# Kernel optimization log

Hardware: AMD Instinct MI355X
Metric: run time of the kernel (lower is better)

The kernel has to match this reference:

```python
import jax, jax.numpy as jnp
import numpy as np

B, S, DIM, H, DH = 1, 4096, 2048, 16, 128
EPS = 1e-5


def setup_inputs() -> dict:
    key = jax.random.key(0)
    ks = jax.random.split(key, 16)
    sc = 0.02
    inp = {
        'hidden_states': jax.random.normal(ks[0], (B, S, DIM), jnp.float32),
        'freqs_cos': jax.random.uniform(ks[1], (1, S, 1, DH), jnp.float32),
        'freqs_sin': jax.random.uniform(ks[2], (1, S, 1, DH), jnp.float32),
        'Wq': jax.random.normal(ks[3], (DIM, DIM), jnp.float32) * sc,
        'bq': jax.random.normal(ks[4], (DIM,), jnp.float32) * sc,
        'Wk': jax.random.normal(ks[5], (DIM, DIM), jnp.float32) * sc,
        'bk': jax.random.normal(ks[6], (DIM,), jnp.float32) * sc,
        'Wv': jax.random.normal(ks[7], (DIM, DIM), jnp.float32) * sc,
        'bv': jax.random.normal(ks[8], (DIM,), jnp.float32) * sc,
        'Wo': jax.random.normal(ks[9], (DIM, DIM), jnp.float32) * sc,
        'bo': jax.random.normal(ks[10], (DIM,), jnp.float32) * sc,
        'gq': jnp.ones((DIM,), jnp.float32),
        'gk': jnp.ones((DIM,), jnp.float32),
    }
    return inp


def _rmsnorm(x, g):
    var = jnp.mean(jnp.square(x), axis=-1, keepdims=True)
    return x * jax.lax.rsqrt(var + EPS) * g


def _apply_rope(x, freqs_cos, freqs_sin):
    # x: [B,S,H,DH]; interleaved rotary as in WanAttnProcessor
    x1 = x[..., 0::2]
    x2 = x[..., 1::2]
    cos = freqs_cos[..., 0::2]
    sin = freqs_sin[..., 1::2]
    o1 = x1 * cos - x2 * sin
    o2 = x1 * sin + x2 * cos
    return jnp.stack([o1, o2], axis=-1).reshape(x.shape)


def reference(hidden_states, freqs_cos, freqs_sin, Wq, bq, Wk, bk, Wv, bv, Wo, bo, gq, gk):
    q = hidden_states @ Wq + bq
    k = hidden_states @ Wk + bk
    v = hidden_states @ Wv + bv
    q = _rmsnorm(q, gq)
    k = _rmsnorm(k, gk)
    q = q.reshape(B, S, H, DH)
    k = k.reshape(B, S, H, DH)
    v = v.reshape(B, S, H, DH)
    q = _apply_rope(q, freqs_cos, freqs_sin)
    k = _apply_rope(k, freqs_cos, freqs_sin)
    scale = 1.0 / np.sqrt(DH).astype(np.float32)
    scores = jnp.einsum('bqhd,bkhd->bhqk', q, k) * scale
    attn = jax.nn.softmax(scores, axis=-1)
    out = jnp.einsum('bhqk,bkhd->bqhd', attn, v)
    out = out.reshape(B, S, H * DH)
    return out @ Wo + bo
```

## Files before the change

### kernel.cpp

```cpp
#include <hip/hip_runtime.h>
#include <hip/hip_bf16.h>

#define SEQ 4096
#define DIMC 2048
#define NH 16
#define DHD 128

typedef short s8v __attribute__((ext_vector_type(8)));
typedef float f4v __attribute__((ext_vector_type(4)));
typedef __bf16 bf8 __attribute__((ext_vector_type(8)));
typedef float f4 __attribute__((ext_vector_type(4)));
typedef float f16v __attribute__((ext_vector_type(16)));
typedef int i4v __attribute__((ext_vector_type(4)));

typedef __attribute__((address_space(3))) void lds_t;
typedef __attribute__((address_space(1))) void gbl_t;

__device__ __attribute__((aligned(256))) short g_h[(size_t)SEQ * DIMC];
__device__ __attribute__((aligned(256))) short g_q[(size_t)SEQ * DIMC];
__device__ __attribute__((aligned(256))) short g_k[(size_t)SEQ * DIMC];
__device__ __attribute__((aligned(256))) short g_v[(size_t)SEQ * DIMC];
__device__ __attribute__((aligned(256))) short g_vt[(size_t)DIMC * SEQ];
__device__ __attribute__((aligned(256))) short g_wt[4][(size_t)DIMC * DIMC];

__device__ __forceinline__ float b2f(short s) {
    union { unsigned u; float f; } v;
    v.u = ((unsigned)(unsigned short)s) << 16;
    return v.f;
}
__device__ __forceinline__ short f2b(float f) {
    union { float f; unsigned u; } v;
    v.f = f;
    unsigned b = v.u;
    b += 0x7FFFu + ((b >> 16) & 1u);
    return (short)(b >> 16);
}
__device__ __forceinline__ f4 mfma16(bf8 a, bf8 b, f4 c) {
    return __builtin_amdgcn_mfma_f32_16x16x32_bf16(a, b, c, 0, 0, 0);
}
__device__ __forceinline__ f16v mfma32(bf8 a, bf8 b, f16v c) {
    return __builtin_amdgcn_mfma_f32_32x32x16_bf16(a, b, c, 0, 0, 0);
}
__device__ __forceinline__ void gl_lds16(const short* g, short* l) {
    __builtin_amdgcn_global_load_lds((gbl_t*)g, (lds_t*)l, 16, 0, 0);
}
__device__ __forceinline__ void plane32_swap(int& a, int& b) {
    asm("v_permlane32_swap_b32 %0, %1" : "+v"(a), "+v"(b));
}
__device__ __forceinline__ int pk2b(float a, float b) {
    int r;
    asm("v_cvt_pk_bf16_f32 %0, %1, %2" : "=v"(r) : "v"(a), "v"(b));
    return r;
}
__device__ __forceinline__ float fexp2(float x) {
#if __has_builtin(__builtin_amdgcn_exp2f)
    return __builtin_amdgcn_exp2f(x);
#else
    float r;
    asm("v_exp_f32 %0, %1" : "=v"(r) : "v"(x));
    return r;
#endif
}

__global__ __launch_bounds__(256) void conv_h(const float* __restrict__ src) {
    size_t i = ((size_t)blockIdx.x * 256 + threadIdx.x) * 8;
    f4v u0 = *reinterpret_cast<const f4v*>(src + i);
    f4v u1 = *reinterpret_cast<const f4v*>(src + i + 4);
    s8v t;
    for (int j = 0; j < 4; ++j) { t[j] = f2b(u0[j]); t[4 + j] = f2b(u1[j]); }
    *reinterpret_cast<s8v*>(g_h + i) = t;
}

__global__ __launch_bounds__(256) void prep_w(const float* __restrict__ W0,
                                              const float* __restrict__ W1,
                                              const float* __restrict__ W2,
                                              const float* __restrict__ W3) {
    __shared__ __attribute__((aligned(16))) float t[64][64];
    const int z = blockIdx.z;
    const float* W = (z == 0) ? W0 : (z == 1) ? W1 : (z == 2) ? W2 : W3;
    short* WT = g_wt[z];
    const int r0 = blockIdx.y * 64, c0 = blockIdx.x * 64;
    const int tid = threadIdx.x;
    for (int i = 0; i < 4; ++i) {
        int slot = tid + i * 256;
        int r = slot >> 4, c4 = (slot & 15) * 4;
        int pb = ((c4 >> 3) + (r >> 3)) & 7;
        *reinterpret_cast<f4v*>(&t[r][pb * 8 + (c4 & 7)]) =
            *reinterpret_cast<const f4v*>(&W[(size_t)(r0 + r) * DIMC + c0 + c4]);
    }
    __syncthreads();
    for (int i = 0; i < 2; ++i) {
        int slot = tid + i * 256;
        int n = slot >> 3, k8 = (slot & 7) * 8;
        int pb = ((n >> 3) + (slot & 7)) & 7;
        s8v o;
        for (int j = 0; j < 8; ++j) o[j] = f2b(t[k8 + j][pb * 8 + (n & 7)]);
        *reinterpret_cast<s8v*>(&WT[(size_t)(c0 + n) * DIMC + r0 + k8]) = o;
    }
}

template <int DSTF>
__device__ __forceinline__ void gemm_body(const short* __restrict__ X,
                                          const short* __restrict__ Bw,
                                          const float* __restrict__ bias,
                                          short* __restrict__ Yb,
                                          float* __restrict__ Yf,
                                          int bm, int bn) {
    __shared__ __attribute__((aligned(16))) short As[128 * 32];
    __shared__ __attribute__((aligned(16))) short Bs[128 * 32];
    const int tid = threadIdx.x;
    const int w = tid >> 6, lane = tid & 63;
    const int l16 = lane & 15, quad = lane >> 4;
    const int wm = w & 1, wn = w >> 1;

    f4 acc[4][4];
    for (int mi = 0; mi < 4; ++mi)
        for (int ni = 0; ni < 4; ++ni) acc[mi][ni] = (f4)0.0f;

    const int s0 = tid, s1 = tid + 256;
    const int ra0 = s0 >> 2, ca0 = (s0 & 3) * 8;
    const int ra1 = s1 >> 2, ca1 = (s1 & 3) * 8;
    const size_t xo0 = (size_t)(bm * 128 + ra0) * DIMC + ca0;
    const size_t xo1 = (size_t)(bm * 128 + ra1) * DIMC + ca1;
    const size_t bo0 = (size_t)(bn * 128 + ra0) * DIMC + ca0;
    const size_t bo1 = (size_t)(bn * 128 + ra1) * DIMC + ca1;
    short* lda0 = As + (size_t)(0 * 256 + w * 64) * 8;
    short* lda1 = As + (size_t)(1 * 256 + w * 64) * 8;
    short* ldb0 = Bs + (size_t)(0 * 256 + w * 64) * 8;
    short* ldb1 = Bs + (size_t)(1 * 256 + w * 64) * 8;

    for (int kb = 0; kb < DIMC; kb += 32) {
        __syncthreads();
        gl_lds16(X + xo0 + kb, lda0);
        gl_lds16(X + xo1 + kb, lda1);
        gl_lds16(Bw + bo0 + kb, ldb0);
        gl_lds16(Bw + bo1 + kb, ldb1);
        __syncthreads();
        bf8 af[4], bfr[4];
        for (int mi = 0; mi < 4; ++mi)
            af[mi] = *reinterpret_cast<const bf8*>(As + (wm * 64 + mi * 16 + l16) * 32 + quad * 8);
        for (int ni = 0; ni < 4; ++ni)
            bfr[ni] = *reinterpret_cast<const bf8*>(Bs + (wn * 64 + ni * 16 + l16) * 32 + quad * 8);
        for (int mi = 0; mi < 4; ++mi)
            for (int ni = 0; ni < 4; ++ni)
                acc[mi][ni] = mfma16(af[mi], bfr[ni], acc[mi][ni]);
    }

    for (int ni = 0; ni < 4; ++ni) {
        int col = bn * 128 + wn * 64 + ni * 16 + l16;
        float bcol = bias[col];
        for (int mi = 0; mi < 4; ++mi) {
            int row = bm * 128 + wm * 64 + mi * 16 + quad * 4;
            for (int r = 0; r < 4; ++r) {
                if (DSTF)
                    Yf[(size_t)(row + r) * DIMC + col] = acc[mi][ni][r] + bcol;
                else
                    Yb[(size_t)(row + r) * DIMC + col] = f2b(acc[mi][ni][r] + bcol);
            }
        }
    }
}

__global__ __launch_bounds__(256, 2) void gemm_qkv(const float* __restrict__ bq,
                                                   const float* __restrict__ bk,
                                                   const float* __restrict__ bv) {
    const int z = blockIdx.z;
    const float* bias = (z == 0) ? bq : (z == 1) ? bk : bv;
    short* Y = (z == 0) ? g_q : (z == 1) ? g_k : g_v;
    gemm_body<0>(g_h, g_wt[z], bias, Y, nullptr, blockIdx.y, blockIdx.x);
}

__global__ __launch_bounds__(256, 2) void gemm_o(const float* __restrict__ bias,
                                                 float* __restrict__ Yf) {
    gemm_body<1>(g_q, g_wt[3], bias, nullptr, Yf, blockIdx.y, blockIdx.x);
}

__global__ __launch_bounds__(256) void rmsnorm_rope(const float* __restrict__ gq,
                                                    const float* __restrict__ gk,
                                                    const float* __restrict__ fc,
                                                    const float* __restrict__ fs) {
    __shared__ float partial[4];
    const int s = blockIdx.x;
    const int which = blockIdx.y;
    short* x = which ? g_k : g_q;
    const float* g = which ? gk : gq;
    const int tid = threadIdx.x;
    const int d0 = tid * 8;

    s8v xv = *reinterpret_cast<const s8v*>(&x[(size_t)s * DIMC + d0]);
    float xf[8];
    float ssq = 0.0f;
    for (int j = 0; j < 8; ++j) { xf[j] = b2f(xv[j]); ssq += xf[j] * xf[j]; }
    for (int off = 32; off; off >>= 1) ssq += __shfl_down(ssq, off);
    if ((tid & 63) == 0) partial[tid >> 6] = ssq;
    __syncthreads();
    float tot = partial[0] + partial[1] + partial[2] + partial[3];
    float rs = rsqrtf(tot * (1.0f / (float)DIMC) + 1e-5f);
    if (which == 0) rs *= 0.12751744f;

    f4v g0 = *reinterpret_cast<const f4v*>(&g[d0]);
    f4v g1 = *reinterpret_cast<const f4v*>(&g[d0 + 4]);
    float xn[8];
    for (int j = 0; j < 4; ++j) { xn[j] = xf[j] * rs * g0[j]; xn[4 + j] = xf[4 + j] * rs * g1[j]; }

    s8v ov;
    for (int p = 0; p < 4; ++p) {
        int e = d0 + 2 * p;
        int hd = e & (DHD - 1);
        float c = fc[(size_t)s * DHD + hd];
        float sn = fs[(size_t)s * DHD + hd + 1];
        float x1 = xn[2 * p], x2 = xn[2 * p + 1];
        ov[2 * p]     = f2b(x1 * c - x2 * sn);
        ov[2 * p + 1] = f2b(x1 * sn + x2 * c);
    }
    *reinterpret_cast<s8v*>(&x[(size_t)s * DIMC + d0]) = ov;
}

__global__ __launch_bounds__(256) void transpose_v() {
    __shared__ __attribute__((aligned(16))) short t[64][64];
    const int h = blockIdx.z, dt = blockIdx.y, st = blockIdx.x;
    const int tid = threadIdx.x;
    const short* src = g_v + (size_t)st * 64 * DIMC + h * DHD + dt * 64;
    for (int i = 0; i < 2; ++i) {
        int slot = tid + i * 256;
        int s = slot >> 3, db = slot & 7;
        int pb = (db + (s >> 3)) & 7;
        *reinterpret_cast<s8v*>(&t[s][pb * 8]) =
            *reinterpret_cast<const s8v*>(src + (size_t)s * DIMC + db * 8);
    }
    __syncthreads();
    short* dst = g_vt + (size_t)(h * DHD + dt * 64) * SEQ + st * 64;
    for (int i = 0; i < 2; ++i) {
        int slot = tid + i * 256;
        int d = slot >> 3, sb = (slot & 7) * 8;
        int pb = ((d >> 3) + (slot & 7)) & 7;
        s8v o;
        for (int j = 0; j < 8; ++j) o[j] = t[sb + j][pb * 8 + (d & 7)];
        *reinterpret_cast<s8v*>(dst + (size_t)d * SEQ + sb) = o;
    }
}

__global__ __launch_bounds__(256, 2) void attn_k() {
    __shared__ __attribute__((aligned(16))) short Ks0[2][64 * 128];
    __shared__ __attribute__((aligned(16))) short Vt0[2][128 * 64];

    const int h = blockIdx.y;
    const int q0 = blockIdx.x * 128;
    const int tid = threadIdx.x;
    const int w = tid >> 6, lane = tid & 63;
    const int l32 = lane & 31, hf = lane >> 5;
    const int l16 = lane & 15;
    const int cbase = hf + l16;
    const int khl = hf + l32;

    bf8 qf[8];
    {
        const short* qb = g_q + (size_t)(q0 + w * 32 + l32) * DIMC + h * DHD + hf * 8;
#pragma unroll
        for (int dc = 0; dc < 8; ++dc)
            qf[dc] = *reinterpret_cast<const bf8*>(qb + dc * 16);
    }

    f16v of[4];
#pragma unroll
    for (int i = 0; i < 4; ++i) of[i] = (f16v)0.0f;
    f16v lacc = (f16v)0.0f;
    const f16v fz = (f16v)0.0f;

    s8v ob;
#pragma unroll
    for (int j = 0; j < 8; ++j) ob[j] = (short)0x3F80;
    const bf8 vones = __builtin_bit_cast(bf8, ob);

    const short* Kbase = g_k + h * DHD;
    const short* Vbase = g_vt + (size_t)h * DHD * SEQ;

    const short* kp[4];
    const short* vp[4];
#pragma unroll
    for (int i = 0; i < 4; ++i) {
        int s = tid + i * 256;
        int krow = s >> 4, kcb = ((s & 15) - krow) & 15;
        int vd = s >> 3, vkb = ((s & 7) - vd) & 7;
        kp[i] = Kbase + (size_t)krow * DIMC + kcb * 8;
        vp[i] = Vbase + (size_t)vd * SEQ + vkb * 8;
    }

#pragma unroll
    for (int i = 0; i < 4; ++i) {
        gl_lds16(kp[i], &Ks0[0][(size_t)(i * 256 + w * 64) * 8]);
        kp[i] += (size_t)64 * DIMC;
    }
#pragma unroll
    for (int i = 0; i < 4; ++i) {
        gl_lds16(vp[i], &Vt0[0][(size_t)(i * 256 + w * 64) * 8]);
        vp[i] += 64;
    }

    auto softmax_pack = [&](const f16v& sa, bf8& paA, bf8& paB) {
        int wv[8];
#pragma unroll
        for (int t = 0; t < 8; ++t)
            wv[t] = pk2b(fexp2(sa[2 * t]), fexp2(sa[2 * t + 1]));
        int a0 = wv[0], b0 = wv[2]; plane32_swap(a0, b0);
        int a1 = wv[1], b1 = wv[3]; plane32_swap(a1, b1);
        int a2 = wv[4], b2 = wv[6]; plane32_swap(a2, b2);
        int a3 = wv[5], b3 = wv[7]; plane32_swap(a3, b3);
        i4v p0 = {a0, a1, b0, b1};
        i4v p1 = {a2, a3, b2, b3};
        paA = __builtin_bit_cast(bf8, p0);
        paB = __builtin_bit_cast(bf8, p1);
    };

    for (int kt = 0; kt < SEQ; kt += 64) {
        const int cur = (kt >> 6) & 1;
        if (kt + 64 < SEQ) {
            const int nxt = cur ^ 1;
#pragma unroll
            for (int i = 0; i < 4; ++i) {
                gl_lds16(kp[i], &Ks0[nxt][(size_t)(i * 256 + w * 64) * 8]);
                kp[i] += (size_t)64 * DIMC;
            }
#pragma unroll
            for (int i = 0; i < 4; ++i) {
                gl_lds16(vp[i], &Vt0[nxt][(size_t)(i * 256 + w * 64) * 8]);
                vp[i] += 64;
            }
            asm volatile("s_waitcnt vmcnt(8)" ::: "memory");
        } else {
            asm volatile("s_waitcnt vmcnt(0)" ::: "memory");
        }
        __builtin_amdgcn_sched_barrier(0);
        __builtin_amdgcn_s_barrier();
        __builtin_amdgcn_sched_barrier(0);

        const short* Ks = Ks0[cur];
        const short* Vt = Vt0[cur];

        const short* krb0 = Ks + l32 * 128;
        const short* krb1 = Ks + (32 + l32) * 128;
        f16v sa0, sa1;
        {
            bf8 k0 = *reinterpret_cast<const bf8*>(krb0 + ((cbase & 15) << 3));
            bf8 k1 = *reinterpret_cast<const bf8*>(krb1 + ((cbase & 15) << 3));
            sa0 = mfma32(k0, qf[0], fz);
            sa1 = mfma32(k1, qf[0], fz);
        }
#pragma unroll
        for (int dc = 1; dc < 8; ++dc) {
            const int cs = ((dc * 2 + cbase) & 15) << 3;
            bf8 k0 = *reinterpret_cast<const bf8*>(krb0 + cs);
            sa0 = mfma32(k0, qf[dc], sa0);
            bf8 k1 = *reinterpret_cast<const bf8*>(krb1 + cs);
            sa1 = mfma32(k1, qf[dc], sa1);
        }

        bf8 p00, p01;
        softmax_pack(sa0, p00, p01);
        lacc = mfma32(p00, vones, lacc);
        lacc = mfma32(p01, vones, lacc);
#pragma unroll
        for (int kp2 = 0; kp2 < 2; ++kp2) {
            bf8 pa = kp2 ? p01 : p00;
#pragma unroll
            for (int dcb = 0; dcb < 4; ++dcb) {
                bf8 vf = *reinterpret_cast<const bf8*>(
                    Vt + (dcb * 32 + l32) * 64 + (((kp2 * 2 + khl) & 7) << 3));
                of[dcb] = mfma32(pa, vf, of[dcb]);
            }
        }

        bf8 p10, p11;
        softmax_pack(sa1, p10, p11);
        lacc = mfma32(p10, vones, lacc);
        lacc = mfma32(p11, vones, lacc);
#pragma unroll
        for (int kp2 = 0; kp2 < 2; ++kp2) {
            bf8 pa = kp2 ? p11 : p10;
#pragma unroll
            for (int dcb = 0; dcb < 4; ++dcb) {
                bf8 vf = *reinterpret_cast<const bf8*>(
                    Vt + (dcb * 32 + l32) * 64 + (((4 + kp2 * 2 + khl) & 7) << 3));
                of[dcb] = mfma32(pa, vf, of[dcb]);
            }
        }

        __builtin_amdgcn_s_barrier();
        __builtin_amdgcn_sched_barrier(0);
    }

#pragma unroll
    for (int r = 0; r < 16; ++r) {
        float iv = 1.0f / lacc[r];
        int row = q0 + w * 32 + (r & 3) + 8 * (r >> 2) + 4 * hf;
#pragma unroll
        for (int dcb = 0; dcb < 4; ++dcb)
            g_q[(size_t)row * DIMC + h * DHD + dcb * 32 + l32] = f2b(of[dcb][r] * iv);
    }
}

extern "C" void kernel_launch(void* const* d_in, const int* in_sizes, int n_in,
                              void* d_out, int out_size, void* d_ws, size_t ws_size,
                              hipStream_t stream) {
    const float* hidden = (const float*)d_in[0];
    const float* fc = (const float*)d_in[1];
    const float* fs = (const float*)d_in[2];
    const float* Wq = (const float*)d_in[3];
    const float* bq = (const float*)d_in[4];
    const float* Wk = (const float*)d_in[5];
    const float* bk = (const float*)d_in[6];
    const float* Wv = (const float*)d_in[7];
    const float* bv = (const float*)d_in[8];
    const float* Wo = (const float*)d_in[9];
    const float* bo = (const float*)d_in[10];
    const float* gq = (const float*)d_in[11];
    const float* gk = (const float*)d_in[12];

    dim3 blk(256);
    conv_h<<<dim3(4096), blk, 0, stream>>>(hidden);
    prep_w<<<dim3(32, 32, 4), blk, 0, stream>>>(Wq, Wk, Wv, Wo);
    gemm_qkv<<<dim3(16, 32, 3), blk, 0, stream>>>(bq, bk, bv);
    rmsnorm_rope<<<dim3(SEQ, 2), blk, 0, stream>>>(gq, gk, fc, fs);
    transpose_v<<<dim3(64, 2, NH), blk, 0, stream>>>();
    attn_k<<<dim3(32, NH), blk, 0, stream>>>();
    gemm_o<<<dim3(16, 32), blk, 0, stream>>>(bo, (float*)d_out);
}
```

Measured before the change: 515.6 us.

## Rewrite GEMMs as 8-wave 256x128 tiles with triple-buffered async LDS pipeline

Replaces the 128x128, K=32, single-buffered GEMM body with a 512-thread 256x128 tile using K=64 steps. It triple-buffers the LDS and issues global-to-LDS loads two stages ahead, interleaving them with MFMA quarters. It also adds an XOR-style swizzle to avoid LDS bank conflicts and uses setprio to favour the MFMA bursts. The goal is to hide memory latency and cut the per-iteration syncthreads stalls, at the cost of much higher LDS use (about 144KB per block) and more complex wait and barrier bookkeeping.

```diff
diff --git a/kernel.cpp b/kernel.cpp
--- a/kernel.cpp
+++ b/kernel.cpp
@@ -100,79 +100,150 @@
 }
 
 template <int DSTF>
-__device__ __forceinline__ void gemm_body(const short* __restrict__ X,
-                                          const short* __restrict__ Bw,
-                                          const float* __restrict__ bias,
-                                          short* __restrict__ Yb,
-                                          float* __restrict__ Yf,
-                                          int bm, int bn) {
-    __shared__ __attribute__((aligned(16))) short As[128 * 32];
-    __shared__ __attribute__((aligned(16))) short Bs[128 * 32];
+__device__ __forceinline__ void gemm8_body(const short* __restrict__ X,
+                                           const short* __restrict__ Bw,
+                                           const float* __restrict__ bias,
+                                           short* __restrict__ Yb,
+                                           float* __restrict__ Yf,
+                                           int bm, int bn) {
+    __shared__ __attribute__((aligned(16))) short Al[3][256 * 64];
+    __shared__ __attribute__((aligned(16))) short Bl[3][128 * 64];
     const int tid = threadIdx.x;
     const int w = tid >> 6, lane = tid & 63;
     const int l16 = lane & 15, quad = lane >> 4;
-    const int wm = w & 1, wn = w >> 1;
+    const int wm = w & 3, wn = w >> 2;
+
+    const int row0 = tid >> 3, cp0 = tid & 7;
+    const int gch = (cp0 - row0) & 7;
+    const short* srcA = X + (size_t)(bm * 256 + row0) * DIMC + gch * 8;
+    const short* srcB = Bw + (size_t)(bn * 128 + row0) * DIMC + gch * 8;
+
+    int offA[2][2][2], offB[2][2][2];
+#pragma unroll
+    for (int qh = 0; qh < 2; ++qh)
+#pragma unroll
+        for (int fi = 0; fi < 2; ++fi)
+#pragma unroll
+            for (int kh = 0; kh < 2; ++kh) {
+                int g = kh * 4 + quad;
+                int ra = wm * 64 + qh * 32 + fi * 16 + l16;
+                offA[qh][fi][kh] = ra * 64 + (((g + ra) & 7) << 3);
+                int rb = wn * 64 + qh * 32 + fi * 16 + l16;
+                offB[qh][fi][kh] = rb * 64 + (((g + rb) & 7) << 3);
+            }
 
     f4 acc[4][4];
-    for (int mi = 0; mi < 4; ++mi)
-        for (int ni = 0; ni < 4; ++ni) acc[mi][ni] = (f4)0.0f;
-
-    const int s0 = tid, s1 = tid + 256;
-    const int ra0 = s0 >> 2, ca0 = (s0 & 3) * 8;
-    const int ra1 = s1 >> 2, ca1 = (s1 & 3) * 8;
-    const size_t xo0 = (size_t)(bm * 128 + ra0) * DIMC + ca0;
-    const size_t xo1 = (size_t)(bm * 128 + ra1) * DIMC + ca1;
-    const size_t bo0 = (size_t)(bn * 128 + ra0) * DIMC + ca0;
-    const size_t bo1 = (size_t)(bn * 128 + ra1) * DIMC + ca1;
-    short* lda0 = As + (size_t)(0 * 256 + w * 64) * 8;
-    short* lda1 = As + (size_t)(1 * 256 + w * 64) * 8;
-    short* ldb0 = Bs + (size_t)(0 * 256 + w * 64) * 8;
-    short* ldb1 = Bs + (size_t)(1 * 256 + w * 64) * 8;
-
-    for (int kb = 0; kb < DIMC; kb += 32) {
-        __syncthreads();
-        gl_lds16(X + xo0 + kb, lda0);
-        gl_lds16(X + xo1 + kb, lda1);
-        gl_lds16(Bw + bo0 + kb, ldb0);
-        gl_lds16(Bw + bo1 + kb, ldb1);
-        __syncthreads();
-        bf8 af[4], bfr[4];
-        for (int mi = 0; mi < 4; ++mi)
-            af[mi] = *reinterpret_cast<const bf8*>(As + (wm * 64 + mi * 16 + l16) * 32 + quad * 8);
-        for (int ni = 0; ni < 4; ++ni)
-            bfr[ni] = *reinterpret_cast<const bf8*>(Bs + (wn * 64 + ni * 16 + l16) * 32 + quad * 8);
-        for (int mi = 0; mi < 4; ++mi)
-            for (int ni = 0; ni < 4; ++ni)
-                acc[mi][ni] = mfma16(af[mi], bfr[ni], acc[mi][ni]);
-    }
-
-    for (int ni = 0; ni < 4; ++ni) {
-        int col = bn * 128 + wn * 64 + ni * 16 + l16;
+#pragma unroll
+    for (int i = 0; i < 4; ++i)
+#pragma unroll
+        for (int j = 0; j < 4; ++j) acc[i][j] = (f4)0.0f;
+
+    const int NT = DIMC / 64;
+
+#pragma unroll
+    for (int x = 0; x < 2; ++x) {
+        gl_lds16(srcA,                        &Al[x][0] + tid * 8);
+        gl_lds16(srcA + (size_t)64 * DIMC,    &Al[x][0] + (tid + 512) * 8);
+        gl_lds16(srcA + (size_t)128 * DIMC,   &Al[x][0] + 8192 + tid * 8);
+        gl_lds16(srcA + (size_t)192 * DIMC,   &Al[x][0] + 8192 + (tid + 512) * 8);
+        gl_lds16(srcB,                        &Bl[x][0] + tid * 8);
+        gl_lds16(srcB + (size_t)64 * DIMC,    &Bl[x][0] + (tid + 512) * 8);
+        srcA += 64; srcB += 64;
+    }
+    asm volatile("s_waitcnt vmcnt(6)" ::: "memory");
+    __builtin_amdgcn_sched_barrier(0);
+    __builtin_amdgcn_s_barrier();
+
+    int b = 0;
+    for (int t = 0; t < NT; ++t) {
+        const short* Ab = &Al[b][0];
+        const short* Bb = &Bl[b][0];
+        const int sb = (b + 2 >= 3) ? b - 1 : b + 2;
+        short* dA = &Al[sb][0];
+        short* dB = &Bl[sb][0];
+        const bool doStage = (t + 2 < NT);
+
+#pragma unroll
+        for (int q = 0; q < 4; ++q) {
+            const int qm = q & 1, qn = q >> 1;
+            bf8 av[2][2], bv[2][2];
+#pragma unroll
+            for (int fi = 0; fi < 2; ++fi)
+#pragma unroll
+                for (int kh = 0; kh < 2; ++kh) {
+                    av[fi][kh] = *reinterpret_cast<const bf8*>(Ab + offA[qm][fi][kh]);
+                    bv[fi][kh] = *reinterpret_cast<const bf8*>(Bb + offB[qn][fi][kh]);
+                }
+            if (doStage) {
+                if (q == 0) {
+                    gl_lds16(srcA,                      dA + tid * 8);
+                    gl_lds16(srcA + (size_t)64 * DIMC,  dA + (tid + 512) * 8);
+                } else if (q == 1) {
+                    gl_lds16(srcA + (size_t)128 * DIMC, dA + 8192 + tid * 8);
+                    gl_lds16(srcA + (size_t)192 * DIMC, dA + 8192 + (tid + 512) * 8);
+                } else if (q == 2) {
+                    gl_lds16(srcB,                      dB + tid * 8);
+                    gl_lds16(srcB + (size_t)64 * DIMC,  dB + (tid + 512) * 8);
+                }
+            }
+            __builtin_amdgcn_s_barrier();
+            asm volatile("s_waitcnt lgkmcnt(0)" ::: "memory");
+            __builtin_amdgcn_sched_barrier(0);
+            __builtin_amdgcn_s_setprio(1);
+#pragma unroll
+            for (int mi = 0; mi < 2; ++mi)
+#pragma unroll
+                for (int ni = 0; ni < 2; ++ni) {
+                    acc[qm * 2 + mi][qn * 2 + ni] =
+                        mfma16(av[mi][0], bv[ni][0], acc[qm * 2 + mi][qn * 2 + ni]);
+                    acc[qm * 2 + mi][qn * 2 + ni] =
+                        mfma16(av[mi][1], bv[ni][1], acc[qm * 2 + mi][qn * 2 + ni]);
+                }
+            __builtin_amdgcn_s_setprio(0);
+            if (q == 3) {
+                if (t + 1 == NT - 1) {
+                    asm volatile("s_waitcnt vmcnt(0)" ::: "memory");
+                } else {
+                    asm volatile("s_waitcnt vmcnt(6)" ::: "memory");
+                }
+                __builtin_amdgcn_sched_barrier(0);
+            }
+            __builtin_amdgcn_s_barrier();
+        }
+        if (doStage) { srcA += 64; srcB += 64; }
+        b = (b + 1 == 3) ? 0 : b + 1;
+    }
+
+#pragma unroll
+    for (int nf = 0; nf < 4; ++nf) {
+        int col = bn * 128 + wn * 64 + nf * 16 + l16;
         float bcol = bias[col];
-        for (int mi = 0; mi < 4; ++mi) {
-            int row = bm * 128 + wm * 64 + mi * 16 + quad * 4;
+#pragma unroll
+        for (int mf = 0; mf < 4; ++mf) {
+            int row = bm * 256 + wm * 64 + mf * 16 + quad * 4;
+#pragma unroll
             for (int r = 0; r < 4; ++r) {
                 if (DSTF)
-                    Yf[(size_t)(row + r) * DIMC + col] = acc[mi][ni][r] + bcol;
+                    Yf[(size_t)(row + r) * DIMC + col] = acc[mf][nf][r] + bcol;
                 else
-                    Yb[(size_t)(row + r) * DIMC + col] = f2b(acc[mi][ni][r] + bcol);
-            }
-        }
-    }
-}
-
-__global__ __launch_bounds__(256, 2) void gemm_qkv(const float* __restrict__ bq,
+                    Yb[(size_t)(row + r) * DIMC + col] = f2b(acc[mf][nf][r] + bcol);
+            }
+        }
+    }
+}
+
+__global__ __launch_bounds__(512, 2) void gemm_qkv(const float* __restrict__ bq,
                                                    const float* __restrict__ bk,
                                                    const float* __restrict__ bv) {
     const int z = blockIdx.z;
     const float* bias = (z == 0) ? bq : (z == 1) ? bk : bv;
     short* Y = (z == 0) ? g_q : (z == 1) ? g_k : g_v;
-    gemm_body<0>(g_h, g_wt[z], bias, Y, nullptr, blockIdx.y, blockIdx.x);
-}
-
-__global__ __launch_bounds__(256, 2) void gemm_o(const float* __restrict__ bias,
+    gemm8_body<0>(g_h, g_wt[z], bias, Y, nullptr, blockIdx.y, blockIdx.x);
+}
+
+__global__ __launch_bounds__(512, 2) void gemm_o(const float* __restrict__ bias,
                                                  float* __restrict__ Yf) {
-    gemm_body<1>(g_q, g_wt[3], bias, nullptr, Yf, blockIdx.y, blockIdx.x);
+    gemm8_body<1>(g_q, g_wt[3], bias, nullptr, Yf, blockIdx.y, blockIdx.x);
 }
 
 __global__ __launch_bounds__(256) void rmsnorm_rope(const float* __restrict__ gq,
@@ -419,9 +490,9 @@
     dim3 blk(256);
     conv_h<<<dim3(4096), blk, 0, stream>>>(hidden);
     prep_w<<<dim3(32, 32, 4), blk, 0, stream>>>(Wq, Wk, Wv, Wo);
-    gemm_qkv<<<dim3(16, 32, 3), blk, 0, stream>>>(bq, bk, bv);
+    gemm_qkv<<<dim3(16, 16, 3), dim3(512), 0, stream>>>(bq, bk, bv);
     rmsnorm_rope<<<dim3(SEQ, 2), blk, 0, stream>>>(gq, gk, fc, fs);
     transpose_v<<<dim3(64, 2, NH), blk, 0, stream>>>();
     attn_k<<<dim3(32, NH), blk, 0, stream>>>();
-    gemm_o<<<dim3(16, 32), blk, 0, stream>>>(bo, (float*)d_out);
-}
+    gemm_o<<<dim3(16, 16), dim3(512), 0, stream>>>(bo, (float*)d_out);
+}
```

New measurement: 550.5 us. 1.07x slower.
